# Kernel optimization log

Measured on AMD Instinct MI355X. Metric: run time of the kernel, lower is better.

Reference implementation:

```python
import jax, jax.numpy as jnp
import numpy as np

DIM = 192
B, Hr, Wr = 16, 64, 64
T = Hr * Wr


def _depthwise(x, w, pad):
    # x: (B,C,H,W), w: (C,1,kh,kw) depthwise (groups=C)
    return jax.lax.conv_general_dilated(
        x, w, window_strides=(1, 1), padding=((pad, pad), (pad, pad)),
        feature_group_count=x.shape[1],
        dimension_numbers=('NCHW', 'OIHW', 'NCHW'))


def _bi_wkv(w, u, k, v):
    # Bidirectional WKV4 (Vision-RWKV style).
    # k, v: (B,T,C); w, u: (C,) already divided by T by caller.
    ew = jnp.exp(-w)              # per-step decay factor, (C,)
    ek = jnp.exp(k)               # (B,T,C)
    ekv = ek * v
    xs = (jnp.swapaxes(ek, 0, 1), jnp.swapaxes(ekv, 0, 1))  # (T,B,C)
    z = jnp.zeros((k.shape[0], k.shape[2]), k.dtype)

    def step(carry, x):
        a, b = carry              # a: weighted-v sum, b: weight sum
        ekt, ekvt = x
        out = (a, b)              # emit BEFORE update -> exclusive sum
        return (ew * a + ekvt, ew * b + ekt), out

    _, (af, bf) = jax.lax.scan(step, (z, z), xs)               # sums over i<t
    _, (ab, bb) = jax.lax.scan(step, (z, z), xs, reverse=True)  # sums over i>t
    a = jnp.swapaxes(af + ab, 0, 1)   # (B,T,C)
    b = jnp.swapaxes(bf + bb, 0, 1)
    euk = jnp.exp(u + k)              # boost term for i==t
    return (a + euk * v) / (b + euk)


def setup_inputs() -> dict:
    key = jax.random.key(0)
    ks = jax.random.split(key, 12)
    inp = {
        'x': jax.random.normal(ks[0], (B, T, DIM), jnp.float32),
        'w1': jax.random.normal(ks[1], (DIM, 1, 1, 1), jnp.float32) * 0.3,
        'w3': jax.random.normal(ks[2], (DIM, 1, 3, 3), jnp.float32) * 0.1,
        'w5': jax.random.normal(ks[3], (DIM, 1, 5, 5), jnp.float32) * 0.06,
        'alpha': jax.random.normal(ks[4], (4,), jnp.float32) * 0.5,
        'Wk': jax.random.normal(ks[5], (DIM, DIM), jnp.float32) * 0.02,
        'Wv': jax.random.normal(ks[6], (DIM, DIM), jnp.float32) * 0.02,
        'Wr': jax.random.normal(ks[7], (DIM, DIM), jnp.float32) * 0.02,
        'Wo': jax.random.normal(ks[8], (DIM, DIM), jnp.float32) * 0.02,
        'decay': jax.random.normal(ks[9], (DIM,), jnp.float32),
        'boost': jax.random.normal(ks[10], (DIM,), jnp.float32),
        'H': Hr,
        'W': Wr,
    }
    return inp


def reference(x, w1, w3, w5, alpha, Wk, Wv, Wr, Wo, decay, boost, H, W):
    Bn, Tn, C = x.shape
    # OmniShift (training branch): alpha-weighted identity + depthwise 1x1/3x3/5x5
    xi = jnp.transpose(x.reshape(Bn, H, W, C), (0, 3, 1, 2))  # b c h w
    s = (alpha[0] * xi + alpha[1] * _depthwise(xi, w1, 0)
         + alpha[2] * _depthwise(xi, w3, 1) + alpha[3] * _depthwise(xi, w5, 2))
    xs = jnp.transpose(s, (0, 2, 3, 1)).reshape(Bn, Tn, C)    # b (h w) c
    # projections (torch Linear: y = x @ W.T)
    k = jnp.einsum('btc,oc->bto', xs, Wk)
    v = jnp.einsum('btc,oc->bto', xs, Wv)
    sr = jax.nn.sigmoid(jnp.einsum('btc,oc->bto', xs, Wr))
    y = _bi_wkv(decay / Tn, boost / Tn, k, v)
    return jnp.einsum('btc,oc->bto', sr * y, Wo)
```

## Files before the change

### kernel.cpp

```cpp
#include <hip/hip_runtime.h>
#include <hip/hip_bf16.h>
#include <math.h>

#define DIM 192
#define NB  16
#define NH  64
#define NW  64
#define NT  4096

#define BN   48
#define NKG  24

typedef __attribute__((ext_vector_type(8))) short short8;
typedef __attribute__((ext_vector_type(4))) float f32x4;
typedef __attribute__((address_space(3))) void* as3_void;
typedef const __attribute__((address_space(1))) void* as1_cvoid;

__device__ __forceinline__ unsigned short f2bf(float x) {
    unsigned int u = __float_as_uint(x);
    u = u + 0x7fffu + ((u >> 16) & 1u);
    return (unsigned short)(u >> 16);
}
__device__ __forceinline__ float bf2f(unsigned short h) {
    return __uint_as_float(((unsigned int)h) << 16);
}
__device__ __forceinline__ void gload16(const void* g, void* l) {
    __builtin_amdgcn_global_load_lds((as1_cvoid)g, (as3_void)l, 16, 0, 0);
}

__global__ void k_prep(const float* __restrict__ w1, const float* __restrict__ w3,
                       const float* __restrict__ w5, const float* __restrict__ alpha,
                       const float* __restrict__ Wk, const float* __restrict__ Wv,
                       const float* __restrict__ Wr, const float* __restrict__ Wo,
                       float* __restrict__ wc,
                       unsigned short* __restrict__ Whi,
                       unsigned short* __restrict__ Wlo) {
    int bid = blockIdx.x, tid = threadIdx.x;
    if (bid == 0) {
        if (tid < DIM) {
            int c = tid;
            float a0 = alpha[0], a1 = alpha[1], a2 = alpha[2], a3 = alpha[3];
            #pragma unroll
            for (int kh = 0; kh < 5; ++kh)
                #pragma unroll
                for (int kw = 0; kw < 5; ++kw) {
                    float v = a3 * w5[c * 25 + kh * 5 + kw];
                    if (kh >= 1 && kh <= 3 && kw >= 1 && kw <= 3)
                        v += a2 * w3[c * 9 + (kh - 1) * 3 + (kw - 1)];
                    if (kh == 2 && kw == 2)
                        v += a0 + a1 * w1[c];
                    wc[c * 25 + kh * 5 + kw] = v;
                }
        }
        return;
    }
    int e = (bid - 1) * 256 + tid;
    if (e >= 4 * DIM * DIM) return;
    int mat = e / (DIM * DIM);
    int idx = e - mat * DIM * DIM;
    const float* W = (mat == 0) ? Wk : (mat == 1 ? Wv : (mat == 2 ? Wr : Wo));
    float v = W[idx];
    unsigned short h = f2bf(v);
    Whi[e] = h;
    Wlo[e] = f2bf(v - bf2f(h));
}

__global__ __launch_bounds__(192) void k_conv(const float* __restrict__ x,
                                              const float* __restrict__ wc,
                                              unsigned short* __restrict__ xs_hi,
                                              unsigned short* __restrict__ xs_lo) {
    int c  = threadIdx.x;
    int bh = blockIdx.x;
    int b = bh >> 6, h = bh & 63;
    const float* xb = x + (size_t)b * NT * DIM + c;
    size_t obase = ((size_t)b * NT + (size_t)h * NW) * DIM + c;

    float wgt[25];
    #pragma unroll
    for (int j = 0; j < 25; ++j) wgt[j] = wc[c * 25 + j];

    const float* rowp[5];
    bool rok[5];
    #pragma unroll
    for (int dh = 0; dh < 5; ++dh) {
        int hh = h + dh - 2;
        rok[dh] = (hh >= 0 && hh < NH);
        rowp[dh] = xb + (size_t)(rok[dh] ? hh : 0) * NW * DIM;
    }

    float win[5][5];
    #pragma unroll
    for (int dh = 0; dh < 5; ++dh) {
        win[dh][0] = 0.f; win[dh][1] = 0.f; win[dh][2] = 0.f;
        win[dh][3] = rok[dh] ? rowp[dh][(size_t)0 * DIM] : 0.f;
        win[dh][4] = rok[dh] ? rowp[dh][(size_t)1 * DIM] : 0.f;
    }

    for (int w = 0; w < NW; ++w) {
        int wcol = w + 2;
        bool cok = (wcol < NW);
        #pragma unroll
        for (int dh = 0; dh < 5; ++dh) {
            win[dh][0] = win[dh][1];
            win[dh][1] = win[dh][2];
            win[dh][2] = win[dh][3];
            win[dh][3] = win[dh][4];
            win[dh][4] = (rok[dh] && cok) ? rowp[dh][(size_t)wcol * DIM] : 0.f;
        }
        float acc = 0.f;
        #pragma unroll
        for (int dh = 0; dh < 5; ++dh)
            #pragma unroll
            for (int dw = 0; dw < 5; ++dw)
                acc = fmaf(win[dh][dw], wgt[dh * 5 + dw], acc);
        unsigned short hb = f2bf(acc);
        xs_hi[obase + (size_t)w * DIM] = hb;
        xs_lo[obase + (size_t)w * DIM] = f2bf(acc - bf2f(hb));
    }
}


#define LOADA(AH, AL, KC)                                                    \
    {                                                                        \
        _Pragma("unroll")                                                    \
        for (int mf = 0; mf < 4; ++mf) {                                     \
            size_t a = (size_t)(arow + mf * 16) * DIM + (KC) * 32 + kofs;    \
            AH[mf] = *(const short8*)&xs_hi[a];                              \
            AL[mf] = *(const short8*)&xs_lo[a];                              \
        }                                                                    \
    }

#define LOADB(BH, BL, KC)                                                    \
    {                                                                        \
        _Pragma("unroll")                                                    \
        for (int nf = 0; nf < 3; ++nf) {                                     \
            BH[nf] = *(const short8*)&Bs[0][(KC) * 4 + lkg][nf * 16 + l15][0]; \
            BL[nf] = *(const short8*)&Bs[1][(KC) * 4 + lkg][nf * 16 + l15][0]; \
        }                                                                    \
    }

#define COMP(AH, AL, BH, BL)                                                 \
    {                                                                        \
        _Pragma("unroll")                                                    \
        for (int mf = 0; mf < 4; ++mf)                                       \
            _Pragma("unroll")                                                \
            for (int nf = 0; nf < 3; ++nf)                                   \
                acc[mf][nf] = __builtin_amdgcn_mfma_f32_16x16x32_bf16(       \
                    AH[mf], BH[nf], acc[mf][nf], 0, 0, 0);                   \
        _Pragma("unroll")                                                    \
        for (int mf = 0; mf < 4; ++mf)                                       \
            _Pragma("unroll")                                                \
            for (int nf = 0; nf < 3; ++nf)                                   \
                acc[mf][nf] = __builtin_amdgcn_mfma_f32_16x16x32_bf16(       \
                    AH[mf], BL[nf], acc[mf][nf], 0, 0, 0);                   \
        _Pragma("unroll")                                                    \
        for (int mf = 0; mf < 4; ++mf)                                       \
            _Pragma("unroll")                                                \
            for (int nf = 0; nf < 3; ++nf)                                   \
                acc[mf][nf] = __builtin_amdgcn_mfma_f32_16x16x32_bf16(       \
                    AL[mf], BH[nf], acc[mf][nf], 0, 0, 0);                   \
    }

#define FENCE __builtin_amdgcn_sched_barrier(0)

__global__ __launch_bounds__(256, 2) void k_gemm_qkv_ws(
        const unsigned short* __restrict__ xs_hi,
        const unsigned short* __restrict__ xs_lo,
        const unsigned short* __restrict__ Whi,
        const unsigned short* __restrict__ Wlo,
        float* __restrict__ kT, float* __restrict__ vT, float* __restrict__ srT) {
    __shared__ __align__(16) short Bs[2][NKG][BN][8];

    const int tid  = threadIdx.x;
    const int lane = tid & 63;
    const int wid  = tid >> 6;
    const int l15  = lane & 15;
    const int lkg  = lane >> 4;
    const int kofs = lkg * 8;

    const int bid   = blockIdx.x;
    const int xcd   = bid & 7;
    const int ix    = bid >> 3;
    const int mtile = xcd * 32 + ix / 12;
    const int sm    = ix % 12;
    const int slice = sm & 3;
    const int mat   = sm >> 2;
    const int n0    = slice * BN;

    const unsigned short* Wh = Whi + mat * (DIM * DIM);
    const unsigned short* Wl = Wlo + mat * (DIM * DIM);
    float* Out = (mat == 0) ? kT : (mat == 1 ? vT : srT);

    #pragma unroll
    for (int r = 0; r < 9; ++r) {
        int g  = r * 256 + tid;
        int g2 = (g >= 1152) ? g - 1152 : g;
        const unsigned short* src = (g >= 1152) ? Wl : Wh;
        int kg  = g2 / BN;
        int col = g2 - kg * BN;
        int doff = (r * 256 + wid * 64) * 16;
        gload16(src + (size_t)(n0 + col) * DIM + kg * 8, (char*)&Bs[0][0][0][0] + doff);
    }

    const int mbase = mtile * 256 + wid * 64;
    const int arow  = mbase + l15;

    f32x4 acc[4][3];
    #pragma unroll
    for (int i = 0; i < 4; ++i)
        #pragma unroll
        for (int j = 0; j < 3; ++j)
            acc[i][j] = (f32x4){0.f, 0.f, 0.f, 0.f};

    short8 ah0[4], al0[4], ah1[4], al1[4];
    short8 bh0[3], bl0[3], bh1[3], bl1[3];

    LOADA(ah0, al0, 0)
    LOADA(ah1, al1, 1)
    __syncthreads();

    LOADB(bh0, bl0, 0)
    LOADB(bh1, bl1, 1)
    FENCE;
    COMP(ah0, al0, bh0, bl0)
    FENCE;
    LOADA(ah0, al0, 2)
    LOADB(bh0, bl0, 2)
    FENCE;
    COMP(ah1, al1, bh1, bl1)
    FENCE;
    LOADA(ah1, al1, 3)
    LOADB(bh1, bl1, 3)
    FENCE;
    COMP(ah0, al0, bh0, bl0)
    FENCE;
    LOADA(ah0, al0, 4)
    LOADB(bh0, bl0, 4)
    FENCE;
    COMP(ah1, al1, bh1, bl1)
    FENCE;
    LOADA(ah1, al1, 5)
    LOADB(bh1, bl1, 5)
    FENCE;
    COMP(ah0, al0, bh0, bl0)
    FENCE;
    COMP(ah1, al1, bh1, bl1)

    const int b  = mbase >> 12;
    const int tb = (mbase & 4095) + lkg * 4;
    #pragma unroll
    for (int mf = 0; mf < 4; ++mf) {
        int t = tb + mf * 16;
        #pragma unroll
        for (int nf = 0; nf < 3; ++nf) {
            int c = n0 + nf * 16 + l15;
            f32x4 v = acc[mf][nf];
            if (mat == 2) {
                v.x = 1.0f / (1.0f + expf(-v.x));
                v.y = 1.0f / (1.0f + expf(-v.y));
                v.z = 1.0f / (1.0f + expf(-v.z));
                v.w = 1.0f / (1.0f + expf(-v.w));
            }
            *(f32x4*)&Out[((size_t)(b * DIM + c)) * NT + t] = v;
        }
    }
}

__global__ __launch_bounds__(256) void k_wkv(
        const float* __restrict__ kT, const float* __restrict__ vT,
        const float* __restrict__ srT, const float* __restrict__ decay,
        const float* __restrict__ boost, float* __restrict__ zT) {
    __shared__ float sa[256], sb[256];
    int bc = blockIdx.x;
    int c = bc % DIM;
    size_t base = (size_t)bc * NT;
    int tid = threadIdx.x;
    int t0 = tid * 16;

    float w  = decay[c] * (1.0f / 4096.0f);
    float u  = boost[c] * (1.0f / 4096.0f);
    float ew = expf(-w);
    float eu = expf(u);

    float ek[16], ekv[16], vv[16];
    #pragma unroll
    for (int j = 0; j < 16; j += 4) {
        float4 k4 = *(const float4*)&kT[base + t0 + j];
        float4 v4 = *(const float4*)&vT[base + t0 + j];
        ek[j + 0] = expf(k4.x); ek[j + 1] = expf(k4.y);
        ek[j + 2] = expf(k4.z); ek[j + 3] = expf(k4.w);
        vv[j + 0] = v4.x; vv[j + 1] = v4.y; vv[j + 2] = v4.z; vv[j + 3] = v4.w;
        ekv[j + 0] = ek[j + 0] * v4.x; ekv[j + 1] = ek[j + 1] * v4.y;
        ekv[j + 2] = ek[j + 2] * v4.z; ekv[j + 3] = ek[j + 3] * v4.w;
    }

    float r = ew * ew; r = r * r; r = r * r; r = r * r;

    float La = 0.f, Lb = 0.f;
    #pragma unroll
    for (int j = 0; j < 16; ++j) { La = fmaf(ew, La, ekv[j]); Lb = fmaf(ew, Lb, ek[j]); }
    sa[tid] = La; sb[tid] = Lb;
    __syncthreads();
    float f = r;
    for (int d = 1; d < 256; d <<= 1) {
        float ta = (tid >= d) ? sa[tid - d] : 0.f;
        float tb_ = (tid >= d) ? sb[tid - d] : 0.f;
        __syncthreads();
        sa[tid] = fmaf(f, ta, sa[tid]);
        sb[tid] = fmaf(f, tb_, sb[tid]);
        __syncthreads();
        f = f * f;
    }
    float Ca = (tid > 0) ? sa[tid - 1] : 0.f;
    float Cb = (tid > 0) ? sb[tid - 1] : 0.f;
    __syncthreads();

    float Ra = 0.f, Rb = 0.f;
    #pragma unroll
    for (int j = 15; j >= 0; --j) { Ra = fmaf(ew, Ra, ekv[j]); Rb = fmaf(ew, Rb, ek[j]); }
    sa[255 - tid] = Ra; sb[255 - tid] = Rb;
    __syncthreads();
    f = r;
    for (int d = 1; d < 256; d <<= 1) {
        float ta = (tid >= d) ? sa[tid - d] : 0.f;
        float tb_ = (tid >= d) ? sb[tid - d] : 0.f;
        __syncthreads();
        sa[tid] = fmaf(f, ta, sa[tid]);
        sb[tid] = fmaf(f, tb_, sb[tid]);
        __syncthreads();
        f = f * f;
    }
    float Da = (tid < 255) ? sa[254 - tid] : 0.f;
    float Db = (tid < 255) ? sb[254 - tid] : 0.f;

    float ab[16], bb[16];
    {
        float a = Da, bv = Db;
        #pragma unroll
        for (int j = 15; j >= 0; --j) {
            ab[j] = a; bb[j] = bv;
            a  = fmaf(ew, a, ekv[j]);
            bv = fmaf(ew, bv, ek[j]);
        }
    }
    float outv[16];
    {
        float a = Ca, bv = Cb;
        #pragma unroll
        for (int j = 0; j < 16; ++j) {
            float af = a, bf = bv;
            a  = fmaf(ew, a, ekv[j]);
            bv = fmaf(ew, bv, ek[j]);
            float euk = eu * ek[j];
            float num = af + ab[j] + euk * vv[j];
            float den = bf + bb[j] + euk;
            outv[j] = num / den;
        }
    }
    #pragma unroll
    for (int j = 0; j < 16; j += 4) {
        float4 s4 = *(const float4*)&srT[base + t0 + j];
        float4 o;
        o.x = s4.x * outv[j + 0];
        o.y = s4.y * outv[j + 1];
        o.z = s4.z * outv[j + 2];
        o.w = s4.w * outv[j + 3];
        *(float4*)&zT[base + t0 + j] = o;
    }
}


#define OSTAGE(BF, KC)                                                       \
    {                                                                        \
        _Pragma("unroll")                                                    \
        for (int pass = 0; pass < 2; ++pass) {                               \
            int t = stq * 4 + pass * 64;                                     \
            const float* z0 = &zT[((size_t)(b * DIM + (KC) * 32 + cp * 2)) * NT + t0 + t]; \
            float4 v0 = *(const float4*)z0;                                  \
            float4 v1 = *(const float4*)(z0 + NT);                           \
            _Pragma("unroll")                                                \
            for (int j = 0; j < 4; ++j) {                                    \
                float f0 = ((const float*)&v0)[j];                           \
                float f1 = ((const float*)&v1)[j];                           \
                unsigned short h0 = f2bf(f0), h1 = f2bf(f1);                 \
                unsigned int hw = (unsigned int)h0 | ((unsigned int)h1 << 16); \
                unsigned int lw = (unsigned int)f2bf(f0 - bf2f(h0))          \
                                | ((unsigned int)f2bf(f1 - bf2f(h1)) << 16); \
                *(unsigned int*)&Ah[BF][t + j][cp * 2] = hw;                 \
                *(unsigned int*)&Al[BF][t + j][cp * 2] = lw;                 \
            }                                                                \
        }                                                                    \
    }

#define OCOMP(BF, KC)                                                        \
    {                                                                        \
        short8 afh[4], afl[4], bfh[3], bfl[3];                               \
        _Pragma("unroll")                                                    \
        for (int mf = 0; mf < 4; ++mf) {                                     \
            int row = wm * 64 + mf * 16 + l15;                               \
            afh[mf] = *(const short8*)&Ah[BF][row][lkg * 8];                 \
            afl[mf] = *(const short8*)&Al[BF][row][lkg * 8];                 \
        }                                                                    \
        _Pragma("unroll")                                                    \
        for (int nf = 0; nf < 3; ++nf) {                                     \
            size_t wb = (size_t)(n0 + wn * 48 + nf * 16 + l15) * DIM + (KC) * 32 + lkg * 8; \
            bfh[nf] = *(const short8*)&Wohi[wb];                             \
            bfl[nf] = *(const short8*)&Wolo[wb];                             \
        }                                                                    \
        _Pragma("unroll")                                                    \
        for (int mf = 0; mf < 4; ++mf)                                       \
            _Pragma("unroll")                                                \
            for (int nf = 0; nf < 3; ++nf)                                   \
                acc[mf][nf] = __builtin_amdgcn_mfma_f32_16x16x32_bf16(       \
                    afh[mf], bfh[nf], acc[mf][nf], 0, 0, 0);                 \
        _Pragma("unroll")                                                    \
        for (int mf = 0; mf < 4; ++mf)                                       \
            _Pragma("unroll")                                                \
            for (int nf = 0; nf < 3; ++nf)                                   \
                acc[mf][nf] = __builtin_amdgcn_mfma_f32_16x16x32_bf16(       \
                    afh[mf], bfl[nf], acc[mf][nf], 0, 0, 0);                 \
        _Pragma("unroll")                                                    \
        for (int mf = 0; mf < 4; ++mf)                                       \
            _Pragma("unroll")                                                \
            for (int nf = 0; nf < 3; ++nf)                                   \
                acc[mf][nf] = __builtin_amdgcn_mfma_f32_16x16x32_bf16(       \
                    afl[mf], bfh[nf], acc[mf][nf], 0, 0, 0);                 \
    }

__global__ __launch_bounds__(256) void k_gemm_out_mfma(
        const float* __restrict__ zT,
        const unsigned short* __restrict__ Wohi,
        const unsigned short* __restrict__ Wolo,
        float* __restrict__ out) {
    __shared__ __align__(16) unsigned short Ah[2][128][40];
    __shared__ __align__(16) unsigned short Al[2][128][40];

    const int tid  = threadIdx.x;
    const int lane = tid & 63;
    const int wid  = tid >> 6;
    const int wm = wid >> 1, wn = wid & 1;
    const int l15 = lane & 15;
    const int lkg = lane >> 4;
    const int n0 = blockIdx.x * 96;
    const int m0 = (int)blockIdx.y * 128;
    const int b  = m0 >> 12;
    const int t0 = m0 & 4095;

    const int cp  = tid >> 4;
    const int stq = tid & 15;

    f32x4 acc[4][3];
    #pragma unroll
    for (int i = 0; i < 4; ++i)
        #pragma unroll
        for (int j = 0; j < 3; ++j)
            acc[i][j] = (f32x4){0.f, 0.f, 0.f, 0.f};

    OSTAGE(0, 0)
    __syncthreads();
    #pragma unroll
    for (int kc = 0; kc < 6; ++kc) {
        if (kc < 5) OSTAGE((kc + 1) & 1, kc + 1)
        OCOMP(kc & 1, kc)
        __syncthreads();
    }

    #pragma unroll
    for (int mf = 0; mf < 4; ++mf) {
        int trow = m0 + wm * 64 + mf * 16 + lkg * 4;
        #pragma unroll
        for (int nf = 0; nf < 3; ++nf) {
            int ncol = n0 + wn * 48 + nf * 16 + l15;
            #pragma unroll
            for (int j = 0; j < 4; ++j)
                out[(size_t)(trow + j) * DIM + ncol] = acc[mf][nf][j];
        }
    }
}

extern "C" void kernel_launch(void* const* d_in, const int* in_sizes, int n_in,
                              void* d_out, int out_size, void* d_ws, size_t ws_size,
                              hipStream_t stream) {
    const float* x     = (const float*)d_in[0];
    const float* w1    = (const float*)d_in[1];
    const float* w3    = (const float*)d_in[2];
    const float* w5    = (const float*)d_in[3];
    const float* alpha = (const float*)d_in[4];
    const float* Wk    = (const float*)d_in[5];
    const float* Wv    = (const float*)d_in[6];
    const float* Wr    = (const float*)d_in[7];
    const float* Wo    = (const float*)d_in[8];
    const float* decay = (const float*)d_in[9];
    const float* boost = (const float*)d_in[10];
    float* out = (float*)d_out;
    float* ws  = (float*)d_ws;

    const size_t BIG = (size_t)NB * NT * DIM;

    float* wc = ws;
    unsigned short* Whi = (unsigned short*)(ws + 8192);
    unsigned short* Wlo = (unsigned short*)(ws + 81920);
    unsigned short* xs_hi = (unsigned short*)(ws + 155648);
    unsigned short* xs_lo = xs_hi + BIG;
    float* kT  = ws + 12738560;
    float* vT  = kT + BIG;
    float* srT = vT + BIG;
    float* zT  = ws + 155648;

    hipLaunchKernelGGL(k_prep, dim3(577), dim3(256), 0, stream,
                       w1, w3, w5, alpha, Wk, Wv, Wr, Wo, wc, Whi, Wlo);
    hipLaunchKernelGGL(k_conv, dim3(NB * NH), dim3(DIM), 0, stream,
                       x, wc, xs_hi, xs_lo);
    hipLaunchKernelGGL(k_gemm_qkv_ws, dim3(3072), dim3(256), 0, stream,
                       xs_hi, xs_lo, Whi, Wlo, kT, vT, srT);
    hipLaunchKernelGGL(k_wkv, dim3(NB * DIM), dim3(256), 0, stream,
                       kT, vT, srT, decay, boost, zT);
    hipLaunchKernelGGL(k_gemm_out_mfma, dim3(2, 65536 / 128), dim3(256), 0, stream,
                       zT, Whi + 3 * DIM * DIM, Wlo + 3 * DIM * DIM, out);
}
```

Measured before the change: 242.7 us.

## Process two M-tiles per QKV GEMM block to reuse staged weights

Each block of the QKV projection GEMM now computes two consecutive 256-row M tiles. It reuses the weight slice already staged in shared memory and prefetches the second tile's A fragments while the first tile's last MFMAs run. The grid is halved to 1536 blocks and launch bounds are raised to 3 waves per SIMD, which amortises the weight staging and block launch overhead. In exchange the accumulator store sits in the middle of the pipeline, and the tighter register budget may cause spills or serialisation.

Measured after the change: 274.8 us. 13.2% more time.

```diff
diff --git a/kernel.cpp b/kernel.cpp
--- a/kernel.cpp
+++ b/kernel.cpp
@@ -120,11 +120,11 @@
 }
 
 
-#define LOADA(AH, AL, KC)                                                    \
+#define LOADA(AH, AL, ROW, KC)                                               \
     {                                                                        \
         _Pragma("unroll")                                                    \
         for (int mf = 0; mf < 4; ++mf) {                                     \
-            size_t a = (size_t)(arow + mf * 16) * DIM + (KC) * 32 + kofs;    \
+            size_t a = (size_t)((ROW) + mf * 16) * DIM + (KC) * 32 + kofs;   \
             AH[mf] = *(const short8*)&xs_hi[a];                              \
             AL[mf] = *(const short8*)&xs_lo[a];                              \
         }                                                                    \
@@ -161,9 +161,40 @@
                     AL[mf], BH[nf], acc[mf][nf], 0, 0, 0);                   \
     }
 
+#define STOREACC(MB)                                                         \
+    {                                                                        \
+        const int b_  = (MB) >> 12;                                          \
+        const int tb_ = ((MB) & 4095) + lkg * 4;                             \
+        _Pragma("unroll")                                                    \
+        for (int mf = 0; mf < 4; ++mf) {                                     \
+            int t = tb_ + mf * 16;                                           \
+            _Pragma("unroll")                                                \
+            for (int nf = 0; nf < 3; ++nf) {                                 \
+                int c = n0 + nf * 16 + l15;                                  \
+                f32x4 v = acc[mf][nf];                                       \
+                if (mat == 2) {                                              \
+                    v.x = 1.0f / (1.0f + expf(-v.x));                        \
+                    v.y = 1.0f / (1.0f + expf(-v.y));                        \
+                    v.z = 1.0f / (1.0f + expf(-v.z));                        \
+                    v.w = 1.0f / (1.0f + expf(-v.w));                        \
+                }                                                            \
+                *(f32x4*)&Out[((size_t)(b_ * DIM + c)) * NT + t] = v;        \
+            }                                                                \
+        }                                                                    \
+    }
+
+#define ZEROACC                                                              \
+    {                                                                        \
+        _Pragma("unroll")                                                    \
+        for (int i = 0; i < 4; ++i)                                          \
+            _Pragma("unroll")                                                \
+            for (int j = 0; j < 3; ++j)                                      \
+                acc[i][j] = (f32x4){0.f, 0.f, 0.f, 0.f};                     \
+    }
+
 #define FENCE __builtin_amdgcn_sched_barrier(0)
 
-__global__ __launch_bounds__(256, 2) void k_gemm_qkv_ws(
+__global__ __launch_bounds__(256, 3) void k_gemm_qkv_ws(
         const unsigned short* __restrict__ xs_hi,
         const unsigned short* __restrict__ xs_lo,
         const unsigned short* __restrict__ Whi,
@@ -181,7 +212,7 @@
     const int bid   = blockIdx.x;
     const int xcd   = bid & 7;
     const int ix    = bid >> 3;
-    const int mtile = xcd * 32 + ix / 12;
+    const int pair  = ix / 12;
     const int sm    = ix % 12;
     const int slice = sm & 3;
     const int mat   = sm >> 2;
@@ -202,21 +233,19 @@
         gload16(src + (size_t)(n0 + col) * DIM + kg * 8, (char*)&Bs[0][0][0][0] + doff);
     }
 
-    const int mbase = mtile * 256 + wid * 64;
-    const int arow  = mbase + l15;
+    const int mbase0 = (xcd * 32 + pair * 2) * 256 + wid * 64;
+    const int mbase1 = mbase0 + 256;
+    const int arow0  = mbase0 + l15;
+    const int arow1  = mbase1 + l15;
 
     f32x4 acc[4][3];
-    #pragma unroll
-    for (int i = 0; i < 4; ++i)
-        #pragma unroll
-        for (int j = 0; j < 3; ++j)
-            acc[i][j] = (f32x4){0.f, 0.f, 0.f, 0.f};
+    ZEROACC
 
     short8 ah0[4], al0[4], ah1[4], al1[4];
     short8 bh0[3], bl0[3], bh1[3], bl1[3];
 
-    LOADA(ah0, al0, 0)
-    LOADA(ah1, al1, 1)
+    LOADA(ah0, al0, arow0, 0)
+    LOADA(ah1, al1, arow0, 1)
     __syncthreads();
 
     LOADB(bh0, bl0, 0)
@@ -224,46 +253,60 @@
     FENCE;
     COMP(ah0, al0, bh0, bl0)
     FENCE;
-    LOADA(ah0, al0, 2)
+    LOADA(ah0, al0, arow0, 2)
     LOADB(bh0, bl0, 2)
     FENCE;
     COMP(ah1, al1, bh1, bl1)
     FENCE;
-    LOADA(ah1, al1, 3)
+    LOADA(ah1, al1, arow0, 3)
     LOADB(bh1, bl1, 3)
     FENCE;
     COMP(ah0, al0, bh0, bl0)
     FENCE;
-    LOADA(ah0, al0, 4)
+    LOADA(ah0, al0, arow0, 4)
     LOADB(bh0, bl0, 4)
     FENCE;
     COMP(ah1, al1, bh1, bl1)
     FENCE;
-    LOADA(ah1, al1, 5)
+    LOADA(ah1, al1, arow0, 5)
     LOADB(bh1, bl1, 5)
     FENCE;
     COMP(ah0, al0, bh0, bl0)
     FENCE;
+    LOADA(ah0, al0, arow1, 0)
+    LOADB(bh0, bl0, 0)
+    FENCE;
     COMP(ah1, al1, bh1, bl1)
-
-    const int b  = mbase >> 12;
-    const int tb = (mbase & 4095) + lkg * 4;
-    #pragma unroll
-    for (int mf = 0; mf < 4; ++mf) {
-        int t = tb + mf * 16;
-        #pragma unroll
-        for (int nf = 0; nf < 3; ++nf) {
-            int c = n0 + nf * 16 + l15;
-            f32x4 v = acc[mf][nf];
-            if (mat == 2) {
-                v.x = 1.0f / (1.0f + expf(-v.x));
-                v.y = 1.0f / (1.0f + expf(-v.y));
-                v.z = 1.0f / (1.0f + expf(-v.z));
-                v.w = 1.0f / (1.0f + expf(-v.w));
-            }
-            *(f32x4*)&Out[((size_t)(b * DIM + c)) * NT + t] = v;
-        }
-    }
+    FENCE;
+    STOREACC(mbase0)
+    ZEROACC
+    LOADA(ah1, al1, arow1, 1)
+    LOADB(bh1, bl1, 1)
+    FENCE;
+    COMP(ah0, al0, bh0, bl0)
+    FENCE;
+    LOADA(ah0, al0, arow1, 2)
+    LOADB(bh0, bl0, 2)
+    FENCE;
+    COMP(ah1, al1, bh1, bl1)
+    FENCE;
+    LOADA(ah1, al1, arow1, 3)
+    LOADB(bh1, bl1, 3)
+    FENCE;
+    COMP(ah0, al0, bh0, bl0)
+    FENCE;
+    LOADA(ah0, al0, arow1, 4)
+    LOADB(bh0, bl0, 4)
+    FENCE;
+    COMP(ah1, al1, bh1, bl1)
+    FENCE;
+    LOADA(ah1, al1, arow1, 5)
+    LOADB(bh1, bl1, 5)
+    FENCE;
+    COMP(ah0, al0, bh0, bl0)
+    FENCE;
+    COMP(ah1, al1, bh1, bl1)
+    STOREACC(mbase1)
 }
 
 __global__ __launch_bounds__(256) void k_wkv(
@@ -511,7 +554,7 @@
                        w1, w3, w5, alpha, Wk, Wv, Wr, Wo, wc, Whi, Wlo);
     hipLaunchKernelGGL(k_conv, dim3(NB * NH), dim3(DIM), 0, stream,
                        x, wc, xs_hi, xs_lo);
-    hipLaunchKernelGGL(k_gemm_qkv_ws, dim3(3072), dim3(256), 0, stream,
+    hipLaunchKernelGGL(k_gemm_qkv_ws, dim3(1536), dim3(256), 0, stream,
                        xs_hi, xs_lo, Whi, Wlo, kT, vT, srT);
     hipLaunchKernelGGL(k_wkv, dim3(NB * DIM), dim3(256), 0, stream,
                        kT, vT, srT, decay, boost, zT);
```
